# Optimization experiments

Measured on AMD Instinct MI355X. Metric: run time of the kernel, lower is better.

## Reference

```python
import jax, jax.numpy as jnp
import numpy as np

EPS = 1e-5  # F.layer_norm default eps
H = 0.1     # step size h

def mm1(K, x):
    # 1x1 conv1d == channel matmul: K [O,I], x [B,I,M] -> [B,O,M]
    return jnp.einsum('oi,bim->bom', K, x)

def full_ln(x):
    # F.layer_norm(x, x.shape): normalize over ALL elements (incl. batch)
    m = jnp.mean(x)
    v = jnp.mean((x - m) ** 2)
    return (x - m) / jnp.sqrt(v + EPS)

def setup_inputs() -> dict:
    key = jax.random.key(0)
    ks = jax.random.split(key, 12)
    B, nNin, nEin = 1, 16, 16
    nNopen = nEopen = nEhid = nNclose = nEclose = 64
    nlayer, N, E = 4, 20000, 320000
    stdv, stdvp = 0.01, 0.001
    NEf = 2 * nNopen + nEopen   # 192
    Nnf = 2 * nEhid + nNopen    # 192
    return {
        'xn': jax.random.normal(ks[0], (B, nNin, N), jnp.float32),
        'xe': jax.random.normal(ks[1], (B, nEin, E), jnp.float32),
        'iInd': jax.random.randint(ks[2], (E,), 0, N, jnp.int32),
        'jInd': jax.random.randint(ks[3], (E,), 0, N, jnp.int32),
        'KNopen': jax.random.normal(ks[4], (nNopen, nNin), jnp.float32) * stdv,
        'KEopen': jax.random.normal(ks[5], (nEopen, nEin), jnp.float32) * stdv,
        'KNclose': jax.random.normal(ks[6], (nNclose, nNopen), jnp.float32) * stdv,
        'KEclose': jax.random.normal(ks[7], (nEclose, nEopen), jnp.float32) * stdv,
        'KE1': jax.random.uniform(ks[8], (nlayer, nEhid, NEf), jnp.float32) * stdvp,
        'KE2': jax.random.uniform(ks[9], (nlayer, nEhid, nEhid), jnp.float32) * stdvp,
        'KE3': jax.random.uniform(ks[10], (nlayer, nEopen, nEhid), jnp.float32) * stdvp,
        'KN': jax.random.uniform(ks[11], (nlayer, nNopen, Nnf), jnp.float32) * stdvp,
    }

def reference(xn, xe, iInd, jInd, KNopen, KEopen, KNclose, KEclose, KE1, KE2, KE3, KN):
    N = xn.shape[-1]
    xn = mm1(KNopen, xn)
    xe = mm1(KEopen, xe)
    nlayers = KE1.shape[0]
    for i in range(nlayers):
        xi = xn[:, :, iInd]
        xj = xn[:, :, jInd]
        gradX = xi - xj               # Graph.nodeGrad
        intX = 0.5 * (xi + xj)        # Graph.nodeAve
        xec = jnp.concatenate([intX, xe, gradX], axis=1)   # [B, 2*nNopen+nEopen, E]
        xec = jax.nn.relu(full_ln(mm1(KE1[i], xec)))
        xec = jax.nn.relu(full_ln(mm1(KE2[i], xec)))
        z = jnp.zeros(xec.shape[:2] + (N,), xec.dtype)
        divXe = z.at[:, :, iInd].add(xec).at[:, :, jInd].add(-xec)          # Graph.edgeDiv
        intXe = 0.5 * z.at[:, :, iInd].add(xec).at[:, :, jInd].add(xec)     # Graph.edgeAve
        xnc = jnp.concatenate([intXe, xn, divXe], axis=1)   # [B, 2*nEhid+nNopen, N]
        xe = xe + H * mm1(KE3[i], xec)
        xn = xn + H * mm1(KN[i], xnc)
    xn = mm1(KNclose, xn)
    xe = mm1(KEclose, xe)
    return (xn, xe)
```

## Files before the change

### kernel.cpp

```cpp
#include <hip/hip_runtime.h>
#include <math.h>

#define H_COEF 0.1f
#define LN_EPS 1e-5

__device__ __forceinline__ int lds_idx(int c, int el) {
  return (c << 8) + (el ^ c);
}

template <int STRIDE>
__device__ __forceinline__ void mm4(const float* __restrict__ Wr,
                                    const float (&x)[64], float (&acc)[4]) {
#pragma unroll
  for (int k = 0; k < 64; k++) {
    const float xk = x[k];
    acc[0] += Wr[0 * STRIDE + k] * xk;
    acc[1] += Wr[1 * STRIDE + k] * xk;
    acc[2] += Wr[2 * STRIDE + k] * xk;
    acc[3] += Wr[3 * STRIDE + k] * xk;
  }
}

__device__ __forceinline__ void stat_reduce(float s, float ss, double* stat) {
#pragma unroll
  for (int off = 32; off > 0; off >>= 1) {
    s += __shfl_down(s, off);
    ss += __shfl_down(ss, off);
  }
  __shared__ float bs[8], bss[8];
  const int wid = threadIdx.x >> 6;
  const int lane = threadIdx.x & 63;
  if (lane == 0) { bs[wid] = s; bss[wid] = ss; }
  __syncthreads();
  if (threadIdx.x == 0) {
    float S = 0.f, SS = 0.f;
    const int nw = blockDim.x >> 6;
    for (int w = 0; w < nw; w++) { S += bs[w]; SS += bss[w]; }
    atomicAdd(stat, (double)S);
    atomicAdd(stat + 1, (double)SS);
  }
}

__global__ __launch_bounds__(256) void prep_weights_kernel(
    const float* __restrict__ KE1, const float* __restrict__ KN,
    const float* __restrict__ KNopen, const float* __restrict__ KNclose,
    float* __restrict__ WUT, float* __restrict__ WVT, float* __restrict__ WNaT,
    float* __restrict__ WNbT, float* __restrict__ WNcT,
    float* __restrict__ WNopT, float* __restrict__ WNclT, int nlayer) {
  const int idx = blockIdx.x * blockDim.x + threadIdx.x;
  const int total = nlayer * 4096;
  if (idx < total) {
    const int l = idx >> 12;
    const int r = idx & 4095;
    const int k = r >> 6;
    const int c = r & 63;
    const float a = KE1[(size_t)l * 12288 + c * 192 + k];
    const float g = KE1[(size_t)l * 12288 + c * 192 + 128 + k];
    WUT[idx] = 0.5f * a + g;
    WVT[idx] = 0.5f * a - g;
    WNaT[idx] = KN[(size_t)l * 12288 + c * 192 + k];
    WNbT[idx] = KN[(size_t)l * 12288 + c * 192 + 64 + k];
    WNcT[idx] = KN[(size_t)l * 12288 + c * 192 + 128 + k];
  }
  if (idx < 4096) {
    const int k = idx >> 6;
    const int c = idx & 63;
    WNclT[idx] = KNclose[c * 64 + k];
    if (k < 16) WNopT[k * 64 + c] = KNopen[c * 16 + k];
  }
}

__global__ __launch_bounds__(256) void hist_kernel(
    const int* __restrict__ iInd, const int* __restrict__ jInd,
    int* __restrict__ cnt_i, int* __restrict__ cnt_j, int E) {
  const int e = blockIdx.x * blockDim.x + threadIdx.x;
  if (e < E) {
    atomicAdd(&cnt_i[iInd[e]], 1);
    atomicAdd(&cnt_j[jInd[e]], 1);
  }
}

__global__ __launch_bounds__(1024) void scan_kernel(
    const int* __restrict__ cnt_i, const int* __restrict__ cnt_j,
    int* __restrict__ rowptr_i, int* __restrict__ cursor_i,
    int* __restrict__ rowptr_j, int* __restrict__ cursor_j, int N) {
  __shared__ unsigned long long carry;
  __shared__ unsigned long long tmp[1024];
  if (threadIdx.x == 0) carry = 0ull;
  __syncthreads();
  for (int base = 0; base < N; base += 1024) {
    const int idx = base + threadIdx.x;
    unsigned long long v = 0ull;
    if (idx < N)
      v = (unsigned long long)(unsigned)cnt_i[idx] |
          ((unsigned long long)(unsigned)cnt_j[idx] << 32);
    tmp[threadIdx.x] = v;
    unsigned long long acc = v;
    __syncthreads();
    for (int off = 1; off < 1024; off <<= 1) {
      const unsigned long long add =
          (threadIdx.x >= (unsigned)off) ? tmp[threadIdx.x - off] : 0ull;
      __syncthreads();
      acc += add;
      tmp[threadIdx.x] = acc;
      __syncthreads();
    }
    const unsigned long long excl = acc - v + carry;
    if (idx < N) {
      const int lo = (int)(excl & 0xffffffffull);
      const int hi = (int)(excl >> 32);
      rowptr_i[idx] = lo;
      cursor_i[idx] = lo;
      rowptr_j[idx] = hi;
      cursor_j[idx] = hi;
    }
    __syncthreads();
    if (threadIdx.x == 1023) carry += tmp[1023];
    __syncthreads();
  }
  if (threadIdx.x == 0) {
    rowptr_i[N] = (int)(carry & 0xffffffffull);
    rowptr_j[N] = (int)(carry >> 32);
  }
}

__global__ __launch_bounds__(256) void fill_kernel(
    const int* __restrict__ iInd, const int* __restrict__ jInd,
    int* __restrict__ cursor_i, int* __restrict__ cursor_j,
    int* __restrict__ perm_i, int* __restrict__ perm_j, int E) {
  const int e = blockIdx.x * blockDim.x + threadIdx.x;
  if (e < E) {
    perm_i[atomicAdd(&cursor_i[iInd[e]], 1)] = e;
    perm_j[atomicAdd(&cursor_j[jInd[e]], 1)] = e;
  }
}

__global__ __launch_bounds__(256) void open_node_uv_kernel(
    const float* __restrict__ WNopT, const float* __restrict__ xn_in,
    const float* __restrict__ WUT0, const float* __restrict__ WVT0,
    float* __restrict__ xn_node, float* __restrict__ U, float* __restrict__ V,
    int N) {
  const int n = blockIdx.x * 4 + (threadIdx.x >> 6);
  const int c = threadIdx.x & 63;
  if (n >= N) return;
  const float xv = (c < 16) ? xn_in[(size_t)c * N + n] : 0.f;
  float acc = 0.f;
#pragma unroll
  for (int k = 0; k < 16; k++) acc += WNopT[k * 64 + c] * __shfl(xv, k);
  xn_node[(size_t)n * 64 + c] = acc;
  float ua = 0.f, va = 0.f;
#pragma unroll
  for (int k = 0; k < 64; k++) {
    const float xk = __shfl(acc, k);
    ua += WUT0[k * 64 + c] * xk;
    va += WVT0[k * 64 + c] * xk;
  }
  U[(size_t)n * 64 + c] = ua;
  V[(size_t)n * 64 + c] = va;
}

template <bool FIRST>
__global__ __launch_bounds__(256) void edge1_kernel(
    const float* __restrict__ KE1_l, const float* __restrict__ KEopen,
    const float* __restrict__ xe_in, float* __restrict__ xe,
    const float* __restrict__ U, const float* __restrict__ V,
    const int* __restrict__ iInd, const int* __restrict__ jInd,
    float* __restrict__ y, double* __restrict__ stat, int E) {
  __shared__ float sbuf[16384];
  const int t = threadIdx.x;
  const int base = blockIdx.x * 256;
  const int e = base + t;
  const bool full = (base + 256 <= E);
  float s = 0.f, ss = 0.f;
  float xcol[64];
  if (e < E) {
    if (FIRST) {
      float xin[16];
#pragma unroll
      for (int k = 0; k < 16; k++) xin[k] = xe_in[(size_t)k * E + e];
#pragma unroll
      for (int cc = 0; cc < 64; cc++) {
        float a = 0.f;
#pragma unroll
        for (int k = 0; k < 16; k++) a += KEopen[cc * 16 + k] * xin[k];
        xcol[cc] = a;
        xe[(size_t)cc * E + e] = a;
      }
    } else {
#pragma unroll
      for (int k = 0; k < 64; k++) xcol[k] = xe[(size_t)k * E + e];
    }
    const int vi = iInd[e];
    const int vj = jInd[e];
    const float4* Up = (const float4*)(U + (size_t)vi * 64);
    const float4* Vp = (const float4*)(V + (size_t)vj * 64);
#pragma unroll
    for (int cg = 0; cg < 16; cg++) {
      const float4 uq = Up[cg];
      const float4 vq = Vp[cg];
      float acc[4] = {uq.x + vq.x, uq.y + vq.y, uq.z + vq.z, uq.w + vq.w};
      mm4<192>(KE1_l + (cg * 4) * 192 + 64, xcol, acc);
#pragma unroll
      for (int u = 0; u < 4; u++) {
        const float a = acc[u];
        s += a;
        ss += a * a;
        if (full) sbuf[lds_idx(cg * 4 + u, t)] = a;
        else y[(size_t)e * 64 + cg * 4 + u] = a;
      }
    }
  }
  if (full) {
    __syncthreads();
    float4* dst = (float4*)(y + (size_t)base * 64);
#pragma unroll
    for (int it = 0; it < 16; it++) {
      const int f4 = t + it * 256;
      const int el = f4 >> 4;
      const int cb = (f4 & 15) << 2;
      float4 r;
      r.x = sbuf[lds_idx(cb + 0, el)];
      r.y = sbuf[lds_idx(cb + 1, el)];
      r.z = sbuf[lds_idx(cb + 2, el)];
      r.w = sbuf[lds_idx(cb + 3, el)];
      dst[f4] = r;
    }
  }
  stat_reduce(s, ss, stat);
}

__global__ __launch_bounds__(256) void edge2_kernel(
    const float* __restrict__ W, float* __restrict__ y,
    const double* __restrict__ statIn, double* __restrict__ statOut,
    double inv_n, int E) {
  __shared__ float sbuf[16384];
  const int t = threadIdx.x;
  const int base = blockIdx.x * 256;
  const int e = base + t;
  const bool full = (base + 256 <= E);
  float s = 0.f, ss = 0.f;
  if (full) {
    const float4* src = (const float4*)(y + (size_t)base * 64);
#pragma unroll
    for (int it = 0; it < 16; it++) {
      const int f4 = t + it * 256;
      const int el = f4 >> 4;
      const int cb = (f4 & 15) << 2;
      const float4 r = src[f4];
      sbuf[lds_idx(cb + 0, el)] = r.x;
      sbuf[lds_idx(cb + 1, el)] = r.y;
      sbuf[lds_idx(cb + 2, el)] = r.z;
      sbuf[lds_idx(cb + 3, el)] = r.w;
    }
    __syncthreads();
  }
  if (e < E) {
    const double m = statIn[0] * inv_n;
    const double v = statIn[1] * inv_n - m * m;
    const float fm = (float)m;
    const float finv = (float)(1.0 / sqrt(v + LN_EPS));
    float tv[64];
    if (full) {
#pragma unroll
      for (int c = 0; c < 64; c++) {
        const float val = (sbuf[lds_idx(c, t)] - fm) * finv;
        tv[c] = val > 0.f ? val : 0.f;
      }
    } else {
#pragma unroll
      for (int c = 0; c < 64; c++) {
        const float val = (y[(size_t)e * 64 + c] - fm) * finv;
        tv[c] = val > 0.f ? val : 0.f;
      }
    }
#pragma unroll
    for (int cg = 0; cg < 16; cg++) {
      float acc[4] = {0.f, 0.f, 0.f, 0.f};
      mm4<64>(W + (cg * 4) * 64, tv, acc);
#pragma unroll
      for (int u = 0; u < 4; u++) {
        const float a = acc[u];
        s += a;
        ss += a * a;
        if (full) sbuf[lds_idx(cg * 4 + u, t)] = a;
        else y[(size_t)e * 64 + cg * 4 + u] = a;
      }
    }
  }
  if (full) {
    __syncthreads();
    float4* dst = (float4*)(y + (size_t)base * 64);
#pragma unroll
    for (int it = 0; it < 16; it++) {
      const int f4 = t + it * 256;
      const int el = f4 >> 4;
      const int cb = (f4 & 15) << 2;
      float4 r;
      r.x = sbuf[lds_idx(cb + 0, el)];
      r.y = sbuf[lds_idx(cb + 1, el)];
      r.z = sbuf[lds_idx(cb + 2, el)];
      r.w = sbuf[lds_idx(cb + 3, el)];
      dst[f4] = r;
    }
  }
  stat_reduce(s, ss, statOut);
}

__global__ __launch_bounds__(256) void edge3_kernel(
    const float* __restrict__ W, const float* __restrict__ y,
    float* __restrict__ xe, const double* __restrict__ statIn, double inv_n,
    int E) {
  const int e = blockIdx.x * blockDim.x + threadIdx.x;
  if (e >= E) return;
  const double m = statIn[0] * inv_n;
  const double v = statIn[1] * inv_n - m * m;
  const float fm = (float)m;
  const float finv = (float)(1.0 / sqrt(v + LN_EPS));
  float tv[64];
  const float4* yrow = (const float4*)(y + (size_t)e * 64);
#pragma unroll
  for (int q = 0; q < 16; q++) {
    const float4 r = yrow[q];
    const float* rp = (const float*)&r;
#pragma unroll
    for (int u = 0; u < 4; u++) {
      const float val = (rp[u] - fm) * finv;
      tv[q * 4 + u] = val > 0.f ? val : 0.f;
    }
  }
#pragma unroll
  for (int cg = 0; cg < 16; cg++) {
    float acc[4] = {0.f, 0.f, 0.f, 0.f};
    mm4<64>(W + (cg * 4) * 64, tv, acc);
#pragma unroll
    for (int u = 0; u < 4; u++) {
      const size_t off = (size_t)(cg * 4 + u) * E + e;
      xe[off] += H_COEF * acc[u];
    }
  }
}

__global__ __launch_bounds__(256) void close_edge_kernel(
    const float* __restrict__ W, float* __restrict__ x, int M) {
  const int e = blockIdx.x * blockDim.x + threadIdx.x;
  if (e >= M) return;
  float xv[64];
#pragma unroll
  for (int k = 0; k < 64; k++) xv[k] = x[(size_t)k * M + e];
#pragma unroll
  for (int cg = 0; cg < 16; cg++) {
    float acc[4] = {0.f, 0.f, 0.f, 0.f};
    mm4<64>(W + (cg * 4) * 64, xv, acc);
#pragma unroll
    for (int u = 0; u < 4; u++)
      x[(size_t)(cg * 4 + u) * M + e] = acc[u];
  }
}

template <bool FINAL>
__global__ __launch_bounds__(256) void fused_node_kernel(
    const float* __restrict__ y, const int* __restrict__ rowptr_i,
    const int* __restrict__ perm_i, const int* __restrict__ rowptr_j,
    const int* __restrict__ perm_j, const float* __restrict__ WNaT,
    const float* __restrict__ WNbT, const float* __restrict__ WNcT,
    const float* __restrict__ WUTn, const float* __restrict__ WVTn,
    const float* __restrict__ WNclT, float* __restrict__ xn_node,
    float* __restrict__ U, float* __restrict__ V, float* __restrict__ xn_out,
    const double* __restrict__ statIn, double inv_n, int N) {
  const int n = blockIdx.x * 4 + (threadIdx.x >> 6);
  const int c = threadIdx.x & 63;
  if (n >= N) return;
  const double m = statIn[0] * inv_n;
  const double v = statIn[1] * inv_n - m * m;
  const float fm = (float)m;
  const float finv = (float)(1.0 / sqrt(v + LN_EPS));

  float si = 0.f;
  const int ib = rowptr_i[n], ie = rowptr_i[n + 1];
  for (int p = ib; p < ie; ++p) {
    const float val = (y[(size_t)perm_i[p] * 64 + c] - fm) * finv;
    si += val > 0.f ? val : 0.f;
  }
  float sj = 0.f;
  const int jb = rowptr_j[n], je = rowptr_j[n + 1];
  for (int p = jb; p < je; ++p) {
    const float val = (y[(size_t)perm_j[p] * 64 + c] - fm) * finv;
    sj += val > 0.f ? val : 0.f;
  }

  const float xv = xn_node[(size_t)n * 64 + c];
  const float a = 0.5f * (si + sj);
  const float d = si - sj;
  float acc = 0.f;
#pragma unroll
  for (int k = 0; k < 64; k++) {
    const float ak = __shfl(a, k);
    const float xk = __shfl(xv, k);
    const float dk = __shfl(d, k);
    acc += WNaT[k * 64 + c] * ak;
    acc += WNbT[k * 64 + c] * xk;
    acc += WNcT[k * 64 + c] * dk;
  }
  const float xn_new = xv + H_COEF * acc;
  if (FINAL) {
    float o = 0.f;
#pragma unroll
    for (int k = 0; k < 64; k++) o += WNclT[k * 64 + c] * __shfl(xn_new, k);
    xn_out[(size_t)c * N + n] = o;
  } else {
    xn_node[(size_t)n * 64 + c] = xn_new;
    float ua = 0.f, va = 0.f;
#pragma unroll
    for (int k = 0; k < 64; k++) {
      const float xk = __shfl(xn_new, k);
      ua += WUTn[k * 64 + c] * xk;
      va += WVTn[k * 64 + c] * xk;
    }
    U[(size_t)n * 64 + c] = ua;
    V[(size_t)n * 64 + c] = va;
  }
}

extern "C" void kernel_launch(void* const* d_in, const int* in_sizes, int n_in,
                              void* d_out, int out_size, void* d_ws,
                              size_t ws_size, hipStream_t stream) {
  const float* xn_in = (const float*)d_in[0];
  const float* xe_in = (const float*)d_in[1];
  const int* iInd = (const int*)d_in[2];
  const int* jInd = (const int*)d_in[3];
  const float* KNopen = (const float*)d_in[4];
  const float* KEopen = (const float*)d_in[5];
  const float* KNclose = (const float*)d_in[6];
  const float* KEclose = (const float*)d_in[7];
  const float* KE1 = (const float*)d_in[8];
  const float* KE2 = (const float*)d_in[9];
  const float* KE3 = (const float*)d_in[10];
  const float* KN = (const float*)d_in[11];

  const int N = in_sizes[0] / 16;
  const int E = in_sizes[2];
  const int nlayer = in_sizes[8] / (64 * 192);

  float* out = (float*)d_out;
  float* xn_out = out;
  float* xe = out + (size_t)64 * N;

  float* ws = (float*)d_ws;
  float* y = ws;
  float* U = y + (size_t)64 * E;
  float* V = U + (size_t)64 * N;
  float* xn_node = V + (size_t)64 * N;
  float* WUT = xn_node + (size_t)64 * N;
  float* WVT = WUT + (size_t)4096 * nlayer;
  float* WNaT = WVT + (size_t)4096 * nlayer;
  float* WNbT = WNaT + (size_t)4096 * nlayer;
  float* WNcT = WNbT + (size_t)4096 * nlayer;
  float* WNopT = WNcT + (size_t)4096 * nlayer;
  float* WNclT = WNopT + 1024;
  double* stat = (double*)(WNclT + 4096);
  int* cnt_i = (int*)(stat + 4 * nlayer);
  int* cnt_j = cnt_i + N;
  int* rowptr_i = cnt_j + N;
  int* cursor_i = rowptr_i + (N + 1);
  int* rowptr_j = cursor_i + N;
  int* cursor_j = rowptr_j + (N + 1);
  int* perm_i = cursor_j + N;
  int* perm_j = perm_i + E;

  const int be = (E + 255) / 256;
  const int bw = (N + 3) / 4;
  const double inv_n = 1.0 / (64.0 * (double)E);

  hipMemsetAsync(stat, 0, (size_t)nlayer * 4 * sizeof(double), stream);
  hipMemsetAsync(cnt_i, 0, (size_t)2 * N * sizeof(int), stream);

  prep_weights_kernel<<<(nlayer * 4096 + 255) / 256, 256, 0, stream>>>(
      KE1, KN, KNopen, KNclose, WUT, WVT, WNaT, WNbT, WNcT, WNopT, WNclT,
      nlayer);

  hist_kernel<<<be, 256, 0, stream>>>(iInd, jInd, cnt_i, cnt_j, E);
  scan_kernel<<<1, 1024, 0, stream>>>(cnt_i, cnt_j, rowptr_i, cursor_i,
                                      rowptr_j, cursor_j, N);
  fill_kernel<<<be, 256, 0, stream>>>(iInd, jInd, cursor_i, cursor_j, perm_i,
                                      perm_j, E);

  open_node_uv_kernel<<<bw, 256, 0, stream>>>(WNopT, xn_in, WUT, WVT, xn_node,
                                              U, V, N);

  for (int l = 0; l < nlayer; l++) {
    const float* KE1_l = KE1 + (size_t)l * 64 * 192;
    const float* KE2_l = KE2 + (size_t)l * 64 * 64;
    const float* KE3_l = KE3 + (size_t)l * 64 * 64;
    double* st1 = stat + (size_t)l * 4;
    double* st2 = st1 + 2;
    const bool last = (l == nlayer - 1);

    if (l == 0) {
      edge1_kernel<true><<<be, 256, 0, stream>>>(KE1_l, KEopen, xe_in, xe, U,
                                                 V, iInd, jInd, y, st1, E);
    } else {
      edge1_kernel<false><<<be, 256, 0, stream>>>(KE1_l, KEopen, xe_in, xe, U,
                                                  V, iInd, jInd, y, st1, E);
    }
    edge2_kernel<<<be, 256, 0, stream>>>(KE2_l, y, st1, st2, inv_n, E);
    edge3_kernel<<<be, 256, 0, stream>>>(KE3_l, y, xe, st2, inv_n, E);
    if (last) {
      fused_node_kernel<true><<<bw, 256, 0, stream>>>(
          y, rowptr_i, perm_i, rowptr_j, perm_j, WNaT + (size_t)l * 4096,
          WNbT + (size_t)l * 4096, WNcT + (size_t)l * 4096, WUT, WVT, WNclT,
          xn_node, U, V, xn_out, st2, inv_n, N);
    } else {
      fused_node_kernel<false><<<bw, 256, 0, stream>>>(
          y, rowptr_i, perm_i, rowptr_j, perm_j, WNaT + (size_t)l * 4096,
          WNbT + (size_t)l * 4096, WNcT + (size_t)l * 4096,
          WUT + (size_t)(l + 1) * 4096, WVT + (size_t)(l + 1) * 4096, WNclT,
          xn_node, U, V, xn_out, st2, inv_n, N);
    }
  }

  close_edge_kernel<<<be, 256, 0, stream>>>(KEclose, xe, E);
}
```

Before: 2.301 ms.

## Drop LDS staging in edge kernels and unroll node gather loops

Removes the 64KB shared-memory transpose buffers from edge1 and edge2. Each thread now writes and reads its 64-float row directly with float4 accesses, and the kernels carry launch_bounds(256,4) to raise occupancy. The node kernel's CSR gather loops are unrolled by 8 with multiple accumulators to expose more memory-level parallelism. The trade-off is that per-thread row stores are strided across threads (256-byte stride), so global coalescing is worse than the staged LDS writes, and summation order changes slightly.

```diff
diff --git a/kernel.cpp b/kernel.cpp
--- a/kernel.cpp
+++ b/kernel.cpp
@@ -3,10 +3,6 @@
 
 #define H_COEF 0.1f
 #define LN_EPS 1e-5
-
-__device__ __forceinline__ int lds_idx(int c, int el) {
-  return (c << 8) + (el ^ c);
-}
 
 template <int STRIDE>
 __device__ __forceinline__ void mm4(const float* __restrict__ Wr,
@@ -160,20 +156,16 @@
 }
 
 template <bool FIRST>
-__global__ __launch_bounds__(256) void edge1_kernel(
+__global__ __launch_bounds__(256, 4) void edge1_kernel(
     const float* __restrict__ KE1_l, const float* __restrict__ KEopen,
     const float* __restrict__ xe_in, float* __restrict__ xe,
     const float* __restrict__ U, const float* __restrict__ V,
     const int* __restrict__ iInd, const int* __restrict__ jInd,
     float* __restrict__ y, double* __restrict__ stat, int E) {
-  __shared__ float sbuf[16384];
-  const int t = threadIdx.x;
-  const int base = blockIdx.x * 256;
-  const int e = base + t;
-  const bool full = (base + 256 <= E);
+  const int e = blockIdx.x * blockDim.x + threadIdx.x;
   float s = 0.f, ss = 0.f;
-  float xcol[64];
   if (e < E) {
+    float xcol[64];
     if (FIRST) {
       float xin[16];
 #pragma unroll
@@ -194,113 +186,63 @@
     const int vj = jInd[e];
     const float4* Up = (const float4*)(U + (size_t)vi * 64);
     const float4* Vp = (const float4*)(V + (size_t)vj * 64);
+    float4* yrow = (float4*)(y + (size_t)e * 64);
 #pragma unroll
     for (int cg = 0; cg < 16; cg++) {
       const float4 uq = Up[cg];
       const float4 vq = Vp[cg];
       float acc[4] = {uq.x + vq.x, uq.y + vq.y, uq.z + vq.z, uq.w + vq.w};
       mm4<192>(KE1_l + (cg * 4) * 192 + 64, xcol, acc);
-#pragma unroll
-      for (int u = 0; u < 4; u++) {
-        const float a = acc[u];
-        s += a;
-        ss += a * a;
-        if (full) sbuf[lds_idx(cg * 4 + u, t)] = a;
-        else y[(size_t)e * 64 + cg * 4 + u] = a;
-      }
-    }
-  }
-  if (full) {
-    __syncthreads();
-    float4* dst = (float4*)(y + (size_t)base * 64);
-#pragma unroll
-    for (int it = 0; it < 16; it++) {
-      const int f4 = t + it * 256;
-      const int el = f4 >> 4;
-      const int cb = (f4 & 15) << 2;
+      s += acc[0] + acc[1] + acc[2] + acc[3];
+      ss += acc[0] * acc[0] + acc[1] * acc[1] + acc[2] * acc[2] +
+            acc[3] * acc[3];
       float4 r;
-      r.x = sbuf[lds_idx(cb + 0, el)];
-      r.y = sbuf[lds_idx(cb + 1, el)];
-      r.z = sbuf[lds_idx(cb + 2, el)];
-      r.w = sbuf[lds_idx(cb + 3, el)];
-      dst[f4] = r;
+      r.x = acc[0];
+      r.y = acc[1];
+      r.z = acc[2];
+      r.w = acc[3];
+      yrow[cg] = r;
     }
   }
   stat_reduce(s, ss, stat);
 }
 
-__global__ __launch_bounds__(256) void edge2_kernel(
+__global__ __launch_bounds__(256, 4) void edge2_kernel(
     const float* __restrict__ W, float* __restrict__ y,
     const double* __restrict__ statIn, double* __restrict__ statOut,
     double inv_n, int E) {
-  __shared__ float sbuf[16384];
-  const int t = threadIdx.x;
-  const int base = blockIdx.x * 256;
-  const int e = base + t;
-  const bool full = (base + 256 <= E);
+  const int e = blockIdx.x * blockDim.x + threadIdx.x;
   float s = 0.f, ss = 0.f;
-  if (full) {
-    const float4* src = (const float4*)(y + (size_t)base * 64);
-#pragma unroll
-    for (int it = 0; it < 16; it++) {
-      const int f4 = t + it * 256;
-      const int el = f4 >> 4;
-      const int cb = (f4 & 15) << 2;
-      const float4 r = src[f4];
-      sbuf[lds_idx(cb + 0, el)] = r.x;
-      sbuf[lds_idx(cb + 1, el)] = r.y;
-      sbuf[lds_idx(cb + 2, el)] = r.z;
-      sbuf[lds_idx(cb + 3, el)] = r.w;
-    }
-    __syncthreads();
-  }
   if (e < E) {
     const double m = statIn[0] * inv_n;
     const double v = statIn[1] * inv_n - m * m;
     const float fm = (float)m;
     const float finv = (float)(1.0 / sqrt(v + LN_EPS));
     float tv[64];
-    if (full) {
-#pragma unroll
-      for (int c = 0; c < 64; c++) {
-        const float val = (sbuf[lds_idx(c, t)] - fm) * finv;
-        tv[c] = val > 0.f ? val : 0.f;
-      }
-    } else {
-#pragma unroll
-      for (int c = 0; c < 64; c++) {
-        const float val = (y[(size_t)e * 64 + c] - fm) * finv;
-        tv[c] = val > 0.f ? val : 0.f;
+    float4* yrow = (float4*)(y + (size_t)e * 64);
+#pragma unroll
+    for (int q = 0; q < 16; q++) {
+      const float4 r = yrow[q];
+      const float* rp = (const float*)&r;
+#pragma unroll
+      for (int u = 0; u < 4; u++) {
+        const float val = (rp[u] - fm) * finv;
+        tv[q * 4 + u] = val > 0.f ? val : 0.f;
       }
     }
 #pragma unroll
     for (int cg = 0; cg < 16; cg++) {
       float acc[4] = {0.f, 0.f, 0.f, 0.f};
       mm4<64>(W + (cg * 4) * 64, tv, acc);
-#pragma unroll
-      for (int u = 0; u < 4; u++) {
-        const float a = acc[u];
-        s += a;
-        ss += a * a;
-        if (full) sbuf[lds_idx(cg * 4 + u, t)] = a;
-        else y[(size_t)e * 64 + cg * 4 + u] = a;
-      }
-    }
-  }
-  if (full) {
-    __syncthreads();
-    float4* dst = (float4*)(y + (size_t)base * 64);
-#pragma unroll
-    for (int it = 0; it < 16; it++) {
-      const int f4 = t + it * 256;
-      const int el = f4 >> 4;
-      const int cb = (f4 & 15) << 2;
+      s += acc[0] + acc[1] + acc[2] + acc[3];
+      ss += acc[0] * acc[0] + acc[1] * acc[1] + acc[2] * acc[2] +
+            acc[3] * acc[3];
       float4 r;
-      r.x = sbuf[lds_idx(cb + 0, el)];
-      r.y = sbuf[lds_idx(cb + 1, el)];
-      r.z = sbuf[lds_idx(cb + 2, el)];
-      r.w = sbuf[lds_idx(cb + 3, el)];
-      dst[f4] = r;
+      r.x = acc[0];
+      r.y = acc[1];
+      r.z = acc[2];
+      r.w = acc[3];
+      yrow[cg] = r;
     }
   }
   stat_reduce(s, ss, statOut);
@@ -375,17 +317,56 @@
   const float fm = (float)m;
   const float finv = (float)(1.0 / sqrt(v + LN_EPS));
 
-  float si = 0.f;
-  const int ib = rowptr_i[n], ie = rowptr_i[n + 1];
-  for (int p = ib; p < ie; ++p) {
-    const float val = (y[(size_t)perm_i[p] * 64 + c] - fm) * finv;
-    si += val > 0.f ? val : 0.f;
-  }
-  float sj = 0.f;
-  const int jb = rowptr_j[n], je = rowptr_j[n + 1];
-  for (int p = jb; p < je; ++p) {
-    const float val = (y[(size_t)perm_j[p] * 64 + c] - fm) * finv;
-    sj += val > 0.f ? val : 0.f;
+  float si, sj;
+#pragma unroll
+  for (int pass = 0; pass < 2; ++pass) {
+    const int* rowptr = pass ? rowptr_j : rowptr_i;
+    const int* perm = pass ? perm_j : perm_i;
+    const int b = rowptr[n], en = rowptr[n + 1];
+    float s0 = 0.f, s1 = 0.f, s2 = 0.f, s3 = 0.f;
+    int p = b;
+    for (; p + 8 <= en; p += 8) {
+      const int e0 = perm[p + 0], e1 = perm[p + 1];
+      const int e2 = perm[p + 2], e3 = perm[p + 3];
+      const int e4 = perm[p + 4], e5 = perm[p + 5];
+      const int e6 = perm[p + 6], e7 = perm[p + 7];
+      const float v0 = y[(size_t)e0 * 64 + c];
+      const float v1 = y[(size_t)e1 * 64 + c];
+      const float v2 = y[(size_t)e2 * 64 + c];
+      const float v3 = y[(size_t)e3 * 64 + c];
+      const float v4 = y[(size_t)e4 * 64 + c];
+      const float v5 = y[(size_t)e5 * 64 + c];
+      const float v6 = y[(size_t)e6 * 64 + c];
+      const float v7 = y[(size_t)e7 * 64 + c];
+      const float r0 = (v0 - fm) * finv, r1 = (v1 - fm) * finv;
+      const float r2 = (v2 - fm) * finv, r3 = (v3 - fm) * finv;
+      const float r4 = (v4 - fm) * finv, r5 = (v5 - fm) * finv;
+      const float r6 = (v6 - fm) * finv, r7 = (v7 - fm) * finv;
+      s0 += r0 > 0.f ? r0 : 0.f;
+      s1 += r1 > 0.f ? r1 : 0.f;
+      s2 += r2 > 0.f ? r2 : 0.f;
+      s3 += r3 > 0.f ? r3 : 0.f;
+      s0 += r4 > 0.f ? r4 : 0.f;
+      s1 += r5 > 0.f ? r5 : 0.f;
+      s2 += r6 > 0.f ? r6 : 0.f;
+      s3 += r7 > 0.f ? r7 : 0.f;
+    }
+    for (; p + 2 <= en; p += 2) {
+      const int e0 = perm[p + 0], e1 = perm[p + 1];
+      const float v0 = y[(size_t)e0 * 64 + c];
+      const float v1 = y[(size_t)e1 * 64 + c];
+      const float r0 = (v0 - fm) * finv, r1 = (v1 - fm) * finv;
+      s0 += r0 > 0.f ? r0 : 0.f;
+      s1 += r1 > 0.f ? r1 : 0.f;
+    }
+    for (; p < en; ++p) {
+      const float v0 = y[(size_t)perm[p] * 64 + c];
+      const float r0 = (v0 - fm) * finv;
+      s0 += r0 > 0.f ? r0 : 0.f;
+    }
+    const float tot = (s0 + s1) + (s2 + s3);
+    if (pass) sj = tot;
+    else si = tot;
   }
 
   const float xv = xn_node[(size_t)n * 64 + c];
```

Result: slower. 4.773 ms (+107.5%).

## Fuse last-layer edge update into close kernel and unroll node gather loops

Applied to the files above, without the earlier changes.

On the last layer, the KE3 residual update is merged with the KEclose projection in one kernel. This avoids writing xe and reading it back between two separate launches. The CSR gather loops in the node kernel are unrolled by 8 with four independent accumulators, so more loads are in flight at once. The fused close kernel holds two 64-float arrays per thread, which raises register pressure.

```diff
diff --git a/kernel.cpp b/kernel.cpp
--- a/kernel.cpp
+++ b/kernel.cpp
@@ -341,19 +341,45 @@
 }
 
 __global__ __launch_bounds__(256) void close_edge_kernel(
-    const float* __restrict__ W, float* __restrict__ x, int M) {
+    const float* __restrict__ KE3_l, const float* __restrict__ Wcl,
+    const float* __restrict__ y, float* __restrict__ xe,
+    const double* __restrict__ statIn, double inv_n, int E) {
   const int e = blockIdx.x * blockDim.x + threadIdx.x;
-  if (e >= M) return;
+  if (e >= E) return;
+  const double m = statIn[0] * inv_n;
+  const double v = statIn[1] * inv_n - m * m;
+  const float fm = (float)m;
+  const float finv = (float)(1.0 / sqrt(v + LN_EPS));
+  float tv[64];
+  const float4* yrow = (const float4*)(y + (size_t)e * 64);
+#pragma unroll
+  for (int q = 0; q < 16; q++) {
+    const float4 r = yrow[q];
+    const float* rp = (const float*)&r;
+#pragma unroll
+    for (int u = 0; u < 4; u++) {
+      const float val = (rp[u] - fm) * finv;
+      tv[q * 4 + u] = val > 0.f ? val : 0.f;
+    }
+  }
   float xv[64];
-#pragma unroll
-  for (int k = 0; k < 64; k++) xv[k] = x[(size_t)k * M + e];
 #pragma unroll
   for (int cg = 0; cg < 16; cg++) {
     float acc[4] = {0.f, 0.f, 0.f, 0.f};
-    mm4<64>(W + (cg * 4) * 64, xv, acc);
+    mm4<64>(KE3_l + (cg * 4) * 64, tv, acc);
+#pragma unroll
+    for (int u = 0; u < 4; u++) {
+      const int cc = cg * 4 + u;
+      xv[cc] = xe[(size_t)cc * E + e] + H_COEF * acc[u];
+    }
+  }
+#pragma unroll
+  for (int cg = 0; cg < 16; cg++) {
+    float acc[4] = {0.f, 0.f, 0.f, 0.f};
+    mm4<64>(Wcl + (cg * 4) * 64, xv, acc);
 #pragma unroll
     for (int u = 0; u < 4; u++)
-      x[(size_t)(cg * 4 + u) * M + e] = acc[u];
+      xe[(size_t)(cg * 4 + u) * E + e] = acc[u];
   }
 }
 
@@ -375,17 +401,48 @@
   const float fm = (float)m;
   const float finv = (float)(1.0 / sqrt(v + LN_EPS));
 
-  float si = 0.f;
-  const int ib = rowptr_i[n], ie = rowptr_i[n + 1];
-  for (int p = ib; p < ie; ++p) {
-    const float val = (y[(size_t)perm_i[p] * 64 + c] - fm) * finv;
-    si += val > 0.f ? val : 0.f;
-  }
-  float sj = 0.f;
-  const int jb = rowptr_j[n], je = rowptr_j[n + 1];
-  for (int p = jb; p < je; ++p) {
-    const float val = (y[(size_t)perm_j[p] * 64 + c] - fm) * finv;
-    sj += val > 0.f ? val : 0.f;
+  float si, sj;
+#pragma unroll
+  for (int pass = 0; pass < 2; ++pass) {
+    const int* rowptr = pass ? rowptr_j : rowptr_i;
+    const int* perm = pass ? perm_j : perm_i;
+    const int b = rowptr[n], en = rowptr[n + 1];
+    float s0 = 0.f, s1 = 0.f, s2 = 0.f, s3 = 0.f;
+    int p = b;
+    for (; p + 8 <= en; p += 8) {
+      const int e0 = perm[p + 0], e1 = perm[p + 1];
+      const int e2 = perm[p + 2], e3 = perm[p + 3];
+      const int e4 = perm[p + 4], e5 = perm[p + 5];
+      const int e6 = perm[p + 6], e7 = perm[p + 7];
+      const float v0 = y[(size_t)e0 * 64 + c];
+      const float v1 = y[(size_t)e1 * 64 + c];
+      const float v2 = y[(size_t)e2 * 64 + c];
+      const float v3 = y[(size_t)e3 * 64 + c];
+      const float v4 = y[(size_t)e4 * 64 + c];
+      const float v5 = y[(size_t)e5 * 64 + c];
+      const float v6 = y[(size_t)e6 * 64 + c];
+      const float v7 = y[(size_t)e7 * 64 + c];
+      const float r0 = (v0 - fm) * finv, r1 = (v1 - fm) * finv;
+      const float r2 = (v2 - fm) * finv, r3 = (v3 - fm) * finv;
+      const float r4 = (v4 - fm) * finv, r5 = (v5 - fm) * finv;
+      const float r6 = (v6 - fm) * finv, r7 = (v7 - fm) * finv;
+      s0 += r0 > 0.f ? r0 : 0.f;
+      s1 += r1 > 0.f ? r1 : 0.f;
+      s2 += r2 > 0.f ? r2 : 0.f;
+      s3 += r3 > 0.f ? r3 : 0.f;
+      s0 += r4 > 0.f ? r4 : 0.f;
+      s1 += r5 > 0.f ? r5 : 0.f;
+      s2 += r6 > 0.f ? r6 : 0.f;
+      s3 += r7 > 0.f ? r7 : 0.f;
+    }
+    for (; p < en; ++p) {
+      const float v0 = y[(size_t)perm[p] * 64 + c];
+      const float r0 = (v0 - fm) * finv;
+      s0 += r0 > 0.f ? r0 : 0.f;
+    }
+    const float tot = (s0 + s1) + (s2 + s3);
+    if (pass) sj = tot;
+    else si = tot;
   }
 
   const float xv = xn_node[(size_t)n * 64 + c];
@@ -503,20 +560,22 @@
                                                   V, iInd, jInd, y, st1, E);
     }
     edge2_kernel<<<be, 256, 0, stream>>>(KE2_l, y, st1, st2, inv_n, E);
-    edge3_kernel<<<be, 256, 0, stream>>>(KE3_l, y, xe, st2, inv_n, E);
-    if (last) {
-      fused_node_kernel<true><<<bw, 256, 0, stream>>>(
-          y, rowptr_i, perm_i, rowptr_j, perm_j, WNaT + (size_t)l * 4096,
-          WNbT + (size_t)l * 4096, WNcT + (size_t)l * 4096, WUT, WVT, WNclT,
-          xn_node, U, V, xn_out, st2, inv_n, N);
-    } else {
+    if (!last) {
+      edge3_kernel<<<be, 256, 0, stream>>>(KE3_l, y, xe, st2, inv_n, E);
       fused_node_kernel<false><<<bw, 256, 0, stream>>>(
           y, rowptr_i, perm_i, rowptr_j, perm_j, WNaT + (size_t)l * 4096,
           WNbT + (size_t)l * 4096, WNcT + (size_t)l * 4096,
           WUT + (size_t)(l + 1) * 4096, WVT + (size_t)(l + 1) * 4096, WNclT,
           xn_node, U, V, xn_out, st2, inv_n, N);
-    }
-  }
-
-  close_edge_kernel<<<be, 256, 0, stream>>>(KEclose, xe, E);
-}
+    } else {
+      fused_node_kernel<true><<<bw, 256, 0, stream>>>(
+          y, rowptr_i, perm_i, rowptr_j, perm_j, WNaT + (size_t)l * 4096,
+          WNbT + (size_t)l * 4096, WNcT + (size_t)l * 4096, WUT, WVT, WNclT,
+          xn_node, U, V, xn_out, st2, inv_n, N);
+    }
+  }
+
+  close_edge_kernel<<<be, 256, 0, stream>>>(
+      KE3 + (size_t)(nlayer - 1) * 64 * 64, KEclose, y, xe,
+      stat + (size_t)(nlayer - 1) * 4 + 2, inv_n, E);
+}
```

Measured after the change: 2.533 ms. 10.1% more time.
